# Optimization experiments

Measured on AMD Instinct MI355X. Metric: run time of the kernel, lower is better.

Reference implementation:

```python
import jax, jax.numpy as jnp
import numpy as np

B, D_IN, D_OUT = 16384, 2048, 2048
BN_EPS = 1e-5


def setup_inputs() -> dict:
    key = jax.random.key(0)
    ks = jax.random.split(key, 6)
    return {
        "x": jax.random.normal(ks[0], (B, D_IN), dtype=jnp.float32),
        "base_weight": jax.random.normal(ks[1], (D_OUT, D_IN), dtype=jnp.float32) * 0.1,
        "bias": jnp.zeros((D_OUT,), dtype=jnp.float32),
        "center": jax.random.normal(ks[2], (D_IN,), dtype=jnp.float32),
        "sharpness": jnp.ones((D_IN,), dtype=jnp.float32),
        "gamma": jnp.ones((D_OUT,), dtype=jnp.float32),
        "beta": jnp.zeros((D_OUT,), dtype=jnp.float32),
        "top_k": 256,
    }


def reference(x, base_weight, bias, center, sharpness, gamma, beta, top_k):
    # fuzzy membership: sigmoid(sharpness * (x - center))  -> [B, D_in]
    mu = jax.nn.sigmoid(sharpness * (x - center))
    b, d = mu.shape

    # OWA weighted membership: keep top_k memberships, scaled by
    # normalized linspace(1.0, 0.1, top_k) weights; zeros elsewhere.
    order = jnp.argsort(-mu, axis=1)                       # descending sort indices
    sorted_vals = jnp.take_along_axis(mu, order, axis=1)
    w = jnp.linspace(1.0, 0.1, top_k, dtype=mu.dtype)
    w = w / w.sum()
    owa = jnp.zeros_like(mu).at[
        jnp.arange(b)[:, None], order[:, :top_k]
    ].set(w[None, :] * sorted_vals[:, :top_k])

    # per-sample scaled matmul: bmm(W * mu_exp, x) == (owa * x) @ W^T
    out = (owa * x) @ base_weight.T + bias                 # [B, D_out]
    out = jax.nn.relu(out)

    # BatchNorm1d in training mode: batch mean, biased variance
    mean = out.mean(axis=0)
    var = out.var(axis=0)
    y = (out - mean) * jax.lax.rsqrt(var + BN_EPS) * gamma + beta
    return (y, mu)
```

## Files before the change

### kernel.cpp

```cpp
#include <hip/hip_runtime.h>
#include <stdint.h>

#define NB 16384
#define DI 2048
#define DO 2048
#define KTOP 256
#define LIST_CAP 384
#define MT (NB / 256)

typedef __attribute__((ext_vector_type(4))) float f32x4;
typedef __attribute__((ext_vector_type(8))) short s16x8;
typedef __attribute__((ext_vector_type(8))) unsigned short u16x8;

#define OWA_C0 7.10227273e-3f
#define OWA_C1 2.50668449e-5f

__device__ __forceinline__ ushort f2bf(float f) {
  uint32_t u = __float_as_uint(f);
  uint32_t r = (u + 0x7FFFu + ((u >> 16) & 1u)) >> 16;
  return (ushort)r;
}

__device__ __forceinline__ float bf2f(ushort b) {
  return __uint_as_float(((uint32_t)b) << 16);
}

__device__ __forceinline__ void gld_lds16(const void* g, void* l) {
  __builtin_amdgcn_global_load_lds((__attribute__((address_space(1))) void*)g,
                                   (__attribute__((address_space(3))) void*)l,
                                   16, 0, 0);
}

__global__ __launch_bounds__(256) void k_cvt(const float* __restrict__ W,
                                             ushort* __restrict__ Wb) {
  size_t i = ((size_t)blockIdx.x * 256 + threadIdx.x) * 8;
  float4 a = *(const float4*)(W + i);
  float4 b = *(const float4*)(W + i + 4);
  u16x8 o;
  o[0] = f2bf(a.x); o[1] = f2bf(a.y); o[2] = f2bf(a.z); o[3] = f2bf(a.w);
  o[4] = f2bf(b.x); o[5] = f2bf(b.y); o[6] = f2bf(b.z); o[7] = f2bf(b.w);
  *(u16x8*)(Wb + i) = o;
}

__global__ __launch_bounds__(256) void k_topk(
    const float* __restrict__ x, const float* __restrict__ center,
    const float* __restrict__ sharp, float* __restrict__ mu_out,
    ushort* __restrict__ A) {
  __shared__ __align__(16) float w_lds[DI];
  __shared__ uint32_t histR[8 * 256];
  __shared__ uint64_t list[LIST_CAP];
  __shared__ uint32_t babove[256];
  __shared__ uint32_t bcnt[256];
  __shared__ uint32_t pzero[256];
  __shared__ uint32_t scal[8];

  const int t = threadIdx.x;
  const int lane = t & 63;
  const int wv = t >> 6;
  const int row = blockIdx.x;
  const int base = t * 8;

  const float* xr = x + (size_t)row * DI + base;
  float4 xa = *(const float4*)(xr);
  float4 xb = *(const float4*)(xr + 4);
  float4 ca = *(const float4*)(center + base);
  float4 cb = *(const float4*)(center + base + 4);
  float4 sa = *(const float4*)(sharp + base);
  float4 sb = *(const float4*)(sharp + base + 4);

  float xv[8] = {xa.x, xa.y, xa.z, xa.w, xb.x, xb.y, xb.z, xb.w};
  float cv[8] = {ca.x, ca.y, ca.z, ca.w, cb.x, cb.y, cb.z, cb.w};
  float sv[8] = {sa.x, sa.y, sa.z, sa.w, sb.x, sb.y, sb.z, sb.w};
  float muv[8];
  uint32_t bits[8];
#pragma unroll
  for (int e = 0; e < 8; ++e) {
    float s = sv[e] * (xv[e] - cv[e]);
    float m = 1.0f / (1.0f + __expf(-s));
    muv[e] = m;
    bits[e] = __float_as_uint(m);
  }
  if (mu_out) {
    float4 m0; m0.x = muv[0]; m0.y = muv[1]; m0.z = muv[2]; m0.w = muv[3];
    float4 m1; m1.x = muv[4]; m1.y = muv[5]; m1.z = muv[6]; m1.w = muv[7];
    *(float4*)(mu_out + (size_t)row * DI + base) = m0;
    *(float4*)(mu_out + (size_t)row * DI + base + 4) = m1;
  }
  float4 z4; z4.x = z4.y = z4.z = z4.w = 0.f;
  *(float4*)(w_lds + base) = z4;
  *(float4*)(w_lds + base + 4) = z4;
  if (t == 0) scal[3] = 0;
#pragma unroll
  for (int i = 0; i < 8; ++i) histR[t + 256 * i] = 0;
  pzero[t] = 0;

  const uint32_t rep = (uint32_t)(t & 7) * 256u;

  uint32_t nhi = 0;
#pragma unroll
  for (int e = 0; e < 8; ++e) nhi += (bits[e] >> 24) == 0x3Fu;
#pragma unroll
  for (int off = 1; off < 64; off <<= 1) nhi += __shfl_xor(nhi, off);
  if (lane == 0) scal[4 + wv] = nhi;
  __syncthreads();
  const uint32_t c_hi = scal[4] + scal[5] + scal[6] + scal[7];

  uint32_t pfx = 0x3F000000u, krem = KTOP;
  if (c_hi < KTOP) {
#pragma unroll
    for (int e = 0; e < 8; ++e) atomicAdd(&histR[rep + (bits[e] >> 24)], 1u);
    __syncthreads();
    if (wv == 0) {
      uint32_t c0 = 0, c1 = 0, c2 = 0, c3 = 0;
#pragma unroll
      for (int r = 0; r < 8; ++r) {
        const uint32_t* h = &histR[r * 256 + lane * 4];
        c0 += h[0]; c1 += h[1]; c2 += h[2]; c3 += h[3];
      }
      uint32_t s3 = c3, s2 = c2 + s3, s1 = c1 + s2, s0 = c0 + s1;
      uint32_t Tl = s0, suf = s0;
#pragma unroll
      for (int off = 1; off < 64; off <<= 1) {
        uint32_t v = __shfl_down(suf, off);
        if (lane + off < 64) suf += v;
      }
      uint32_t above = suf - Tl;
      uint32_t SS[4] = {s0 + above, s1 + above, s2 + above, s3 + above};
      uint32_t cc[4] = {c0, c1, c2, c3};
#pragma unroll
      for (int j = 0; j < 4; ++j) {
        if (SS[j] >= KTOP && (SS[j] - cc[j]) < KTOP) {
          scal[0] = (uint32_t)(lane * 4 + j);
          scal[1] = SS[j] - cc[j];
        }
      }
    }
    __syncthreads();
    pfx = scal[0] << 24;
    krem = KTOP - scal[1];
#pragma unroll
    for (int i = 0; i < 8; ++i) histR[t + 256 * i] = 0;
    __syncthreads();
  }
  const uint32_t pfxbyte = pfx >> 24;
  const uint32_t nsuper = KTOP - krem;

#pragma unroll
  for (int e = 0; e < 8; ++e) {
    if ((bits[e] >> 24) == pfxbyte)
      atomicAdd(&histR[rep + ((bits[e] >> 16) & 255u)], 1u);
  }
  __syncthreads();
  if (wv == 0) {
    uint32_t c0 = 0, c1 = 0, c2 = 0, c3 = 0;
#pragma unroll
    for (int r = 0; r < 8; ++r) {
      const uint32_t* h = &histR[r * 256 + lane * 4];
      c0 += h[0]; c1 += h[1]; c2 += h[2]; c3 += h[3];
    }
    uint32_t s3 = c3, s2 = c2 + s3, s1 = c1 + s2, s0 = c0 + s1;
    uint32_t Tl = s0, suf = s0;
#pragma unroll
    for (int off = 1; off < 64; off <<= 1) {
      uint32_t v = __shfl_down(suf, off);
      if (lane + off < 64) suf += v;
    }
    uint32_t above = suf - Tl;
    uint32_t SS[4] = {s0 + above, s1 + above, s2 + above, s3 + above};
    uint32_t cc[4] = {c0, c1, c2, c3};
    uint4 ba, bc;
    ba.x = SS[0] - cc[0]; ba.y = SS[1] - cc[1];
    ba.z = SS[2] - cc[2]; ba.w = SS[3] - cc[3];
    bc.x = cc[0]; bc.y = cc[1]; bc.z = cc[2]; bc.w = cc[3];
    *(uint4*)&babove[lane * 4] = ba;
    *(uint4*)&bcnt[lane * 4] = bc;
#pragma unroll
    for (int j = 0; j < 4; ++j) {
      if (SS[j] >= krem && (SS[j] - cc[j]) < krem) {
        scal[0] = (uint32_t)(lane * 4 + j);
      }
    }
  }
  __syncthreads();
  const uint32_t tb = pfx | (scal[0] << 16);

  int lo8[8], hi8[8];
#pragma unroll
  for (int e = 0; e < 8; ++e) {
    lo8[e] = 0; hi8[e] = 0;
    if (bits[e] >= tb) {
      uint64_t key = ((uint64_t)bits[e] << 32) |
                     (uint64_t)(uint32_t)(DI - 1 - (base + e));
      uint32_t lo, hi, slot;
      if ((bits[e] >> 24) == pfxbyte) {
        uint32_t d = (bits[e] >> 16) & 255u;
        uint32_t idx = atomicAdd(&pzero[d], 1u);
        lo = nsuper + babove[d];
        hi = lo + bcnt[d];
        slot = lo + idx;
      } else {
        uint32_t idx = atomicAdd(&scal[3], 1u);
        lo = 0; hi = nsuper; slot = idx;
      }
      if (slot < LIST_CAP) list[slot] = key;
      lo8[e] = (int)lo;
      hi8[e] = (int)(hi > LIST_CAP ? LIST_CAP : hi);
    }
  }
  __syncthreads();

#pragma unroll
  for (int e = 0; e < 8; ++e) {
    if (bits[e] >= tb) {
      uint64_t key = ((uint64_t)bits[e] << 32) |
                     (uint64_t)(uint32_t)(DI - 1 - (base + e));
      int r = lo8[e];
      for (int j = lo8[e]; j < hi8[e]; ++j) r += (int)(list[j] > key);
      if (r < KTOP) w_lds[base + e] = OWA_C0 - OWA_C1 * (float)r;
    }
  }
  __syncthreads();

  u16x8 ov;
#pragma unroll
  for (int e = 0; e < 8; ++e) ov[e] = f2bf(w_lds[base + e] * muv[e] * xv[e]);
  *(u16x8*)(A + (size_t)row * DI + base) = ov;
}

#define HALFS 8192

#define MFMA(a, b, c) __builtin_amdgcn_mfma_f32_16x16x32_bf16(a, b, c, 0, 0, 0)

#define STAGE_A(U, h)                                                       \
  do {                                                                      \
    ushort* sl = lA + (((((U) & 1) << 1) + (h)) * HALFS);                   \
    gld_lds16(pA0 + (size_t)((h) * 128) * DI + (size_t)(U) * 64, sl + d0);  \
    gld_lds16(pA0 + (size_t)((h) * 128 + 64) * DI + (size_t)(U) * 64,       \
              sl + d1);                                                     \
  } while (0)

#define STAGE_B(U, h)                                                       \
  do {                                                                      \
    ushort* sl = lB + (((((U) & 1) << 1) + (h)) * HALFS);                   \
    gld_lds16(pB0 + (size_t)((h) * 128) * DI + (size_t)(U) * 64, sl + d0);  \
    gld_lds16(pB0 + (size_t)((h) * 128 + 64) * DI + (size_t)(U) * 64,       \
              sl + d1);                                                     \
  } while (0)

#define RD_A(BUF, slotp, rowb)                                              \
  do {                                                                      \
    const ushort* rp_ = (slotp) + ((rowb) + fr) * 64;                       \
    BUF[0] = *(const s16x8*)(rp_ + c0);                                     \
    BUF[1] = *(const s16x8*)(rp_ + c1);                                     \
    BUF[2] = *(const s16x8*)(rp_ + 16 * 64 + c0);                           \
    BUF[3] = *(const s16x8*)(rp_ + 16 * 64 + c1);                           \
  } while (0)

#define RD_B(slotp)                                                         \
  do {                                                                      \
    _Pragma("unroll") for (int ni = 0; ni < 4; ++ni) {                      \
      breg[ni][0] = *(const s16x8*)((slotp) + ni * 1024 + boff + c0);       \
      breg[ni][1] = *(const s16x8*)((slotp) + ni * 1024 + boff + c1);       \
    }                                                                       \
  } while (0)

#define MFMA_PHASE(q, BUF)                                                  \
  do {                                                                      \
    __builtin_amdgcn_s_setprio(1);                                          \
    _Pragma("unroll") for (int ni = 0; ni < 4; ++ni) {                      \
      acc[2 * (q)][ni] = MFMA(BUF[0], breg[ni][0], acc[2 * (q)][ni]);       \
      acc[2 * (q)][ni] = MFMA(BUF[1], breg[ni][1], acc[2 * (q)][ni]);       \
      acc[2 * (q) + 1][ni] = MFMA(BUF[2], breg[ni][0], acc[2 * (q) + 1][ni]); \
      acc[2 * (q) + 1][ni] = MFMA(BUF[3], breg[ni][1], acc[2 * (q) + 1][ni]); \
    }                                                                       \
    __builtin_amdgcn_s_setprio(0);                                          \
  } while (0)

#define PHASE(q, RD_STMT, STAGE_STMT, BUF, POST_STMT, TAIL_STMT, LG)        \
  do {                                                                      \
    RD_STMT;                                                                \
    STAGE_STMT;                                                             \
    asm volatile("s_waitcnt lgkmcnt(" LG ")" ::: "memory");                 \
    __builtin_amdgcn_sched_barrier(0);                                      \
    MFMA_PHASE(q, BUF);                                                     \
    POST_STMT;                                                              \
    TAIL_STMT;                                                              \
    __builtin_amdgcn_s_barrier();                                           \
  } while (0)

template <int OB16>
__global__ __launch_bounds__(512, 2) void k_gemm(
    const ushort* __restrict__ A, const ushort* __restrict__ Wb,
    const float* __restrict__ bias, float* __restrict__ outp,
    ushort* __restrict__ outb,
    float* __restrict__ psum, float* __restrict__ psumsq) {
  __shared__ __align__(16) ushort lA[4 * HALFS];
  __shared__ __align__(16) ushort lB[4 * HALFS];

  const int t = threadIdx.x;
  const int lane = t & 63;
  const int wv = t >> 6;
  const int wm = wv >> 2;
  const int wn = wv & 3;
  const int wm32 = wm * 32;
  const int fr = lane & 15;
  const int kg = lane >> 4;
  const int s = fr & 7;

  int bid = blockIdx.x;
  int orig = (bid & 7) * 64 + (bid >> 3);
  const int nb = orig & 7;
  const int mb = orig >> 3;
  const int m0 = mb * 256;
  const int n0 = nb * 256;

  const int srow0 = t >> 3;
  const int scol = ((t & 7) ^ (srow0 & 7)) * 8;
  const ushort* pA0 = A + (size_t)(m0 + srow0) * DI + scol;
  const ushort* pB0 = Wb + (size_t)(n0 + srow0) * DI + scol;
  const int d0 = t * 8;
  const int d1 = (512 + t) * 8;

  f32x4 acc[8][4];
#pragma unroll
  for (int i = 0; i < 8; ++i)
#pragma unroll
    for (int j = 0; j < 4; ++j) acc[i][j] = (f32x4){0.f, 0.f, 0.f, 0.f};

  const int c0 = (kg ^ s) * 8;
  const int c1 = ((4 + kg) ^ s) * 8;
  const int boff = ((wn & 1) * 64 + fr) * 64;

  s16x8 breg[4][2];
  s16x8 bufA_[4], bufB_[4];

  STAGE_B(0, 0); STAGE_B(0, 1);
  STAGE_A(0, 0); STAGE_A(0, 1);
  STAGE_B(1, 0); STAGE_B(1, 1);
  asm volatile("s_waitcnt vmcnt(6)" ::: "memory");
  __builtin_amdgcn_s_barrier();
  RD_B(lB + (wn >> 1) * HALFS);
  RD_A(bufA_, lA, wm32);

#pragma unroll 1
  for (int T = 0; T < 31; ++T) {
    const ushort* lAcur = lA + ((T & 1) << 1) * HALFS;
    const ushort* lAnxt = lA + (((T + 1) & 1) << 1) * HALFS;
    const ushort* sBnxt = lB + ((((T + 1) & 1) << 1) + (wn >> 1)) * HALFS;

    PHASE(0, RD_A(bufB_, lAcur, 64 + wm32), STAGE_A(T + 1, 0), bufA_, ,
          asm volatile("s_waitcnt vmcnt(6)" ::: "memory"), "4");
    PHASE(1, RD_A(bufA_, lAcur + HALFS, wm32), STAGE_A(T + 1, 1), bufB_, , ,
          "4");
    PHASE(2, RD_A(bufB_, lAcur + HALFS, 64 + wm32),
          if (T < 30) STAGE_B(T + 2, 0), bufA_, ,
          if (T < 30) { asm volatile("s_waitcnt vmcnt(4)" ::: "memory"); }
          else { asm volatile("s_waitcnt vmcnt(2)" ::: "memory"); }, "4");
    PHASE(3, RD_A(bufA_, lAnxt, wm32), if (T < 30) STAGE_B(T + 2, 1), bufB_,
          RD_B(sBnxt), , "4");
  }
  {
    const ushort* lAcur = lA + 2 * HALFS;
    PHASE(0, RD_A(bufB_, lAcur, 64 + wm32), , bufA_, ,
          asm volatile("s_waitcnt vmcnt(0)" ::: "memory"), "4");
    PHASE(1, RD_A(bufA_, lAcur + HALFS, wm32), , bufB_, , , "4");
    PHASE(2, RD_A(bufB_, lAcur + HALFS, 64 + wm32), , bufA_, , , "4");
    PHASE(3, , , bufB_, , , "0");
  }

  __syncthreads();
  float* colsum = (float*)lA;
  float* colsq = colsum + 256;
  if (t < 256) { colsum[t] = 0.f; colsq[t] = 0.f; }
  __syncthreads();
#pragma unroll
  for (int ni = 0; ni < 4; ++ni) {
    const int n = n0 + wn * 64 + ni * 16 + fr;
    const float bv = bias[n];
    float cs = 0.f, cq = 0.f;
#pragma unroll
    for (int mi = 0; mi < 8; ++mi) {
      const int rowb = m0 + 64 * (mi >> 1) + wm32 + 16 * (mi & 1) + kg * 4;
      f32x4 v = acc[mi][ni];
#pragma unroll
      for (int r = 0; r < 4; ++r) {
        float zz = fmaxf(v[r] + bv, 0.f);
        if (OB16) outb[(size_t)(rowb + r) * DO + n] = f2bf(zz);
        else      outp[(size_t)(rowb + r) * DO + n] = zz;
        cs += zz;
        cq += zz * zz;
      }
    }
    cs += __shfl_xor(cs, 16); cq += __shfl_xor(cq, 16);
    cs += __shfl_xor(cs, 32); cq += __shfl_xor(cq, 32);
    if (kg == 0) {
      atomicAdd(&colsum[wn * 64 + ni * 16 + fr], cs);
      atomicAdd(&colsq[wn * 64 + ni * 16 + fr], cq);
    }
  }
  __syncthreads();
  if (t < 256) {
    psum[(size_t)mb * DO + n0 + t] = colsum[t];
    psumsq[(size_t)mb * DO + n0 + t] = colsq[t];
  }
}

__global__ __launch_bounds__(256) void k_bnfin(
    const float* __restrict__ psum, const float* __restrict__ psumsq,
    const float* __restrict__ gamma, const float* __restrict__ beta,
    float* __restrict__ scaleA, float* __restrict__ shiftA) {
  int n = blockIdx.x * 256 + threadIdx.x;
  float s = 0.f, q = 0.f;
  for (int r = 0; r < MT; ++r) {
    s += psum[(size_t)r * DO + n];
    q += psumsq[(size_t)r * DO + n];
  }
  float mean = s * (1.0f / (float)NB);
  float var = q * (1.0f / (float)NB) - mean * mean;
  var = fmaxf(var, 0.f);
  float rstd = rsqrtf(var + 1e-5f);
  float sc = gamma[n] * rstd;
  scaleA[n] = sc;
  shiftA[n] = beta[n] - mean * sc;
}

__global__ __launch_bounds__(256) void k_bnapply(float* __restrict__ outp,
                                                 const float* __restrict__ scaleA,
                                                 const float* __restrict__ shiftA) {
  size_t i = ((size_t)blockIdx.x * 256 + threadIdx.x) * 4;
  int n = (int)(i & (DO - 1));
  float4 v = *(float4*)(outp + i);
  float4 sc = *(const float4*)(scaleA + n);
  float4 sh = *(const float4*)(shiftA + n);
  v.x = v.x * sc.x + sh.x;
  v.y = v.y * sc.y + sh.y;
  v.z = v.z * sc.z + sh.z;
  v.w = v.w * sc.w + sh.w;
  *(float4*)(outp + i) = v;
}

__global__ __launch_bounds__(256) void k_bnapply_b16(
    const ushort* __restrict__ outb, float* __restrict__ y,
    const float* __restrict__ scaleA, const float* __restrict__ shiftA) {
  size_t i = ((size_t)blockIdx.x * 256 + threadIdx.x) * 8;
  int n = (int)(i & (DO - 1));
  u16x8 v = *(const u16x8*)(outb + i);
  float4 s0 = *(const float4*)(scaleA + n);
  float4 s1 = *(const float4*)(scaleA + n + 4);
  float4 h0 = *(const float4*)(shiftA + n);
  float4 h1 = *(const float4*)(shiftA + n + 4);
  float4 y0, y1;
  y0.x = bf2f(v[0]) * s0.x + h0.x;
  y0.y = bf2f(v[1]) * s0.y + h0.y;
  y0.z = bf2f(v[2]) * s0.z + h0.z;
  y0.w = bf2f(v[3]) * s0.w + h0.w;
  y1.x = bf2f(v[4]) * s1.x + h1.x;
  y1.y = bf2f(v[5]) * s1.y + h1.y;
  y1.z = bf2f(v[6]) * s1.z + h1.z;
  y1.w = bf2f(v[7]) * s1.w + h1.w;
  *(float4*)(y + i) = y0;
  *(float4*)(y + i + 4) = y1;
}

__global__ __launch_bounds__(256) void k_mu(const float* __restrict__ x,
                                            const float* __restrict__ center,
                                            const float* __restrict__ sharp,
                                            float* __restrict__ mu_out) {
  const int t = threadIdx.x;
  const int row = blockIdx.x;
  const int base = t * 8;
  const float* xr = x + (size_t)row * DI + base;
  float4 xa = *(const float4*)(xr);
  float4 xb = *(const float4*)(xr + 4);
  float4 ca = *(const float4*)(center + base);
  float4 cb = *(const float4*)(center + base + 4);
  float4 sa = *(const float4*)(sharp + base);
  float4 sb = *(const float4*)(sharp + base + 4);
  float xv[8] = {xa.x, xa.y, xa.z, xa.w, xb.x, xb.y, xb.z, xb.w};
  float cv[8] = {ca.x, ca.y, ca.z, ca.w, cb.x, cb.y, cb.z, cb.w};
  float sv[8] = {sa.x, sa.y, sa.z, sa.w, sb.x, sb.y, sb.z, sb.w};
  float mu[8];
#pragma unroll
  for (int e = 0; e < 8; ++e) {
    float s = sv[e] * (xv[e] - cv[e]);
    mu[e] = 1.0f / (1.0f + __expf(-s));
  }
  float4 m0; m0.x = mu[0]; m0.y = mu[1]; m0.z = mu[2]; m0.w = mu[3];
  float4 m1; m1.x = mu[4]; m1.y = mu[5]; m1.z = mu[6]; m1.w = mu[7];
  *(float4*)(mu_out + (size_t)row * DI + base) = m0;
  *(float4*)(mu_out + (size_t)row * DI + base + 4) = m1;
}

extern "C" void kernel_launch(void* const* d_in, const int* in_sizes, int n_in,
                              void* d_out, int out_size, void* d_ws, size_t ws_size,
                              hipStream_t stream) {
  (void)in_sizes; (void)n_in; (void)out_size;
  const float* x = (const float*)d_in[0];
  const float* W = (const float*)d_in[1];
  const float* bias = (const float*)d_in[2];
  const float* center = (const float*)d_in[3];
  const float* sharp = (const float*)d_in[4];
  const float* gamma = (const float*)d_in[5];
  const float* beta = (const float*)d_in[6];

  float* outY = (float*)d_out;
  float* outMu = outY + (size_t)NB * DO;

  const size_t A_BYTES = (size_t)NB * DI * 2;
  const size_t WB_BYTES = (size_t)DO * DI * 2;
  const size_t PS_BYTES = (size_t)MT * DO * 4;
  const size_t SC_BYTES = (size_t)DO * 4;
  const size_t OB_BYTES = (size_t)NB * DO * 2;
  const size_t NEED_BIG = A_BYTES + WB_BYTES + 2 * PS_BYTES + 2 * SC_BYTES;

  char* p = (char*)d_ws;
  bool bigws = (ws_size >= NEED_BIG);
  bool ob16 = (ws_size >= NEED_BIG + OB_BYTES);
  ushort* A;
  if (bigws) { A = (ushort*)p; p += A_BYTES; }
  else       { A = (ushort*)outMu; }
  ushort* Wb = (ushort*)p; p += WB_BYTES;
  float* psum = (float*)p; p += PS_BYTES;
  float* psumsq = (float*)p; p += PS_BYTES;
  float* scaleA = (float*)p; p += SC_BYTES;
  float* shiftA = (float*)p; p += SC_BYTES;
  ushort* outB = (ushort*)p;

  k_cvt<<<dim3((DO * DI) / (256 * 8)), dim3(256), 0, stream>>>(W, Wb);
  k_topk<<<dim3(NB), dim3(256), 0, stream>>>(x, center, sharp,
                                             bigws ? outMu : (float*)nullptr, A);
  if (ob16) {
    k_gemm<1><<<dim3((NB / 256) * (DO / 256)), dim3(512), 0, stream>>>(
        A, Wb, bias, outY, outB, psum, psumsq);
  } else {
    k_gemm<0><<<dim3((NB / 256) * (DO / 256)), dim3(512), 0, stream>>>(
        A, Wb, bias, outY, (ushort*)outY , psum, psumsq);
  }
  k_bnfin<<<dim3(DO / 256), dim3(256), 0, stream>>>(psum, psumsq, gamma, beta,
                                                    scaleA, shiftA);
  if (ob16) {
    k_bnapply_b16<<<dim3((size_t)NB * DO / 8 / 256), dim3(256), 0, stream>>>(
        outB, outY, scaleA, shiftA);
  } else {
    k_bnapply<<<dim3((size_t)NB * DO / 4 / 256), dim3(256), 0, stream>>>(
        outY, scaleA, shiftA);
  }
  if (!bigws) k_mu<<<dim3(NB), dim3(256), 0, stream>>>(x, center, sharp, outMu);
}
```

Measured before the change: 305.8 us.

## Split GEMM tile across 16 waves with 1024-thread blocks

Doubles the GEMM workgroup from 512 to 1024 threads, so each wave computes a 16-row by 64-column slice with half the accumulators and A fragments. Each thread now issues one global-to-LDS load per stage instead of two, and the wait counts are adjusted to match. Column statistics now go into per-wave-row slots in LDS and are summed at the end instead of using LDS atomics. Each phase gains an extra barrier and a full lgkmcnt(0) wait before its MFMAs, which drops the previous A-fragment double-buffering. Occupancy falls to one block per CU, so there is less latency hiding and more synchronisation.

```diff
diff --git a/kernel.cpp b/kernel.cpp
--- a/kernel.cpp
+++ b/kernel.cpp
@@ -235,25 +235,19 @@
   do {                                                                      \
     ushort* sl = lA + (((((U) & 1) << 1) + (h)) * HALFS);                   \
     gld_lds16(pA0 + (size_t)((h) * 128) * DI + (size_t)(U) * 64, sl + d0);  \
-    gld_lds16(pA0 + (size_t)((h) * 128 + 64) * DI + (size_t)(U) * 64,       \
-              sl + d1);                                                     \
   } while (0)
 
 #define STAGE_B(U, h)                                                       \
   do {                                                                      \
     ushort* sl = lB + (((((U) & 1) << 1) + (h)) * HALFS);                   \
     gld_lds16(pB0 + (size_t)((h) * 128) * DI + (size_t)(U) * 64, sl + d0);  \
-    gld_lds16(pB0 + (size_t)((h) * 128 + 64) * DI + (size_t)(U) * 64,       \
-              sl + d1);                                                     \
   } while (0)
 
-#define RD_A(BUF, slotp, rowb)                                              \
+#define RD_A(slotp, rowb)                                                   \
   do {                                                                      \
     const ushort* rp_ = (slotp) + ((rowb) + fr) * 64;                       \
-    BUF[0] = *(const s16x8*)(rp_ + c0);                                     \
-    BUF[1] = *(const s16x8*)(rp_ + c1);                                     \
-    BUF[2] = *(const s16x8*)(rp_ + 16 * 64 + c0);                           \
-    BUF[3] = *(const s16x8*)(rp_ + 16 * 64 + c1);                           \
+    abuf[0] = *(const s16x8*)(rp_ + c0);                                    \
+    abuf[1] = *(const s16x8*)(rp_ + c1);                                    \
   } while (0)
 
 #define RD_B(slotp)                                                         \
@@ -264,32 +258,31 @@
     }                                                                       \
   } while (0)
 
-#define MFMA_PHASE(q, BUF)                                                  \
+#define MFMA_PHASE(q)                                                       \
   do {                                                                      \
     __builtin_amdgcn_s_setprio(1);                                          \
     _Pragma("unroll") for (int ni = 0; ni < 4; ++ni) {                      \
-      acc[2 * (q)][ni] = MFMA(BUF[0], breg[ni][0], acc[2 * (q)][ni]);       \
-      acc[2 * (q)][ni] = MFMA(BUF[1], breg[ni][1], acc[2 * (q)][ni]);       \
-      acc[2 * (q) + 1][ni] = MFMA(BUF[2], breg[ni][0], acc[2 * (q) + 1][ni]); \
-      acc[2 * (q) + 1][ni] = MFMA(BUF[3], breg[ni][1], acc[2 * (q) + 1][ni]); \
+      acc[q][ni] = MFMA(abuf[0], breg[ni][0], acc[q][ni]);                  \
+      acc[q][ni] = MFMA(abuf[1], breg[ni][1], acc[q][ni]);                  \
     }                                                                       \
     __builtin_amdgcn_s_setprio(0);                                          \
   } while (0)
 
-#define PHASE(q, RD_STMT, STAGE_STMT, BUF, POST_STMT, TAIL_STMT, LG)        \
+#define PHASE(q, RD_STMT, STAGE_STMT, POST_STMT, TAIL_STMT)                 \
   do {                                                                      \
     RD_STMT;                                                                \
     STAGE_STMT;                                                             \
-    asm volatile("s_waitcnt lgkmcnt(" LG ")" ::: "memory");                 \
+    __builtin_amdgcn_s_barrier();                                           \
+    asm volatile("s_waitcnt lgkmcnt(0)" ::: "memory");                      \
     __builtin_amdgcn_sched_barrier(0);                                      \
-    MFMA_PHASE(q, BUF);                                                     \
+    MFMA_PHASE(q);                                                          \
     POST_STMT;                                                              \
     TAIL_STMT;                                                              \
     __builtin_amdgcn_s_barrier();                                           \
   } while (0)
 
 template <int OB16>
-__global__ __launch_bounds__(512, 2) void k_gemm(
+__global__ __launch_bounds__(1024) void k_gemm(
     const ushort* __restrict__ A, const ushort* __restrict__ Wb,
     const float* __restrict__ bias, float* __restrict__ outp,
     ushort* __restrict__ outb,
@@ -302,7 +295,7 @@
   const int wv = t >> 6;
   const int wm = wv >> 2;
   const int wn = wv & 3;
-  const int wm32 = wm * 32;
+  const int wm16 = wm * 16;
   const int fr = lane & 15;
   const int kg = lane >> 4;
   const int s = fr & 7;
@@ -319,11 +312,10 @@
   const ushort* pA0 = A + (size_t)(m0 + srow0) * DI + scol;
   const ushort* pB0 = Wb + (size_t)(n0 + srow0) * DI + scol;
   const int d0 = t * 8;
-  const int d1 = (512 + t) * 8;
-
-  f32x4 acc[8][4];
-#pragma unroll
-  for (int i = 0; i < 8; ++i)
+
+  f32x4 acc[4][4];
+#pragma unroll
+  for (int i = 0; i < 4; ++i)
 #pragma unroll
     for (int j = 0; j < 4; ++j) acc[i][j] = (f32x4){0.f, 0.f, 0.f, 0.f};
 
@@ -332,46 +324,43 @@
   const int boff = ((wn & 1) * 64 + fr) * 64;
 
   s16x8 breg[4][2];
-  s16x8 bufA_[4], bufB_[4];
+  s16x8 abuf[2];
 
   STAGE_B(0, 0); STAGE_B(0, 1);
   STAGE_A(0, 0); STAGE_A(0, 1);
   STAGE_B(1, 0); STAGE_B(1, 1);
-  asm volatile("s_waitcnt vmcnt(6)" ::: "memory");
+  asm volatile("s_waitcnt vmcnt(3)" ::: "memory");
   __builtin_amdgcn_s_barrier();
   RD_B(lB + (wn >> 1) * HALFS);
-  RD_A(bufA_, lA, wm32);
 
 #pragma unroll 1
   for (int T = 0; T < 31; ++T) {
     const ushort* lAcur = lA + ((T & 1) << 1) * HALFS;
-    const ushort* lAnxt = lA + (((T + 1) & 1) << 1) * HALFS;
     const ushort* sBnxt = lB + ((((T + 1) & 1) << 1) + (wn >> 1)) * HALFS;
 
-    PHASE(0, RD_A(bufB_, lAcur, 64 + wm32), STAGE_A(T + 1, 0), bufA_, ,
-          asm volatile("s_waitcnt vmcnt(6)" ::: "memory"), "4");
-    PHASE(1, RD_A(bufA_, lAcur + HALFS, wm32), STAGE_A(T + 1, 1), bufB_, , ,
-          "4");
-    PHASE(2, RD_A(bufB_, lAcur + HALFS, 64 + wm32),
-          if (T < 30) STAGE_B(T + 2, 0), bufA_, ,
-          if (T < 30) { asm volatile("s_waitcnt vmcnt(4)" ::: "memory"); }
-          else { asm volatile("s_waitcnt vmcnt(2)" ::: "memory"); }, "4");
-    PHASE(3, RD_A(bufA_, lAnxt, wm32), if (T < 30) STAGE_B(T + 2, 1), bufB_,
-          RD_B(sBnxt), , "4");
+    PHASE(0, RD_A(lAcur, wm16), STAGE_A(T + 1, 0), ,
+          asm volatile("s_waitcnt vmcnt(3)" ::: "memory"));
+    PHASE(1, RD_A(lAcur, 64 + wm16), STAGE_A(T + 1, 1), , );
+    PHASE(2, RD_A(lAcur + HALFS, wm16), if (T < 30) STAGE_B(T + 2, 0), ,
+          if (T < 30) { asm volatile("s_waitcnt vmcnt(2)" ::: "memory"); }
+          else { asm volatile("s_waitcnt vmcnt(1)" ::: "memory"); });
+    PHASE(3, RD_A(lAcur + HALFS, 64 + wm16), if (T < 30) STAGE_B(T + 2, 1),
+          RD_B(sBnxt), );
   }
   {
     const ushort* lAcur = lA + 2 * HALFS;
-    PHASE(0, RD_A(bufB_, lAcur, 64 + wm32), , bufA_, ,
-          asm volatile("s_waitcnt vmcnt(0)" ::: "memory"), "4");
-    PHASE(1, RD_A(bufA_, lAcur + HALFS, wm32), , bufB_, , , "4");
-    PHASE(2, RD_A(bufB_, lAcur + HALFS, 64 + wm32), , bufA_, , , "4");
-    PHASE(3, , , bufB_, , , "0");
-  }
-
-  __syncthreads();
-  float* colsum = (float*)lA;
-  float* colsq = colsum + 256;
-  if (t < 256) { colsum[t] = 0.f; colsq[t] = 0.f; }
+    PHASE(0, RD_A(lAcur, wm16), , ,
+          asm volatile("s_waitcnt vmcnt(0)" ::: "memory"));
+    PHASE(1, RD_A(lAcur, 64 + wm16), , , );
+    PHASE(2, RD_A(lAcur + HALFS, wm16), , , );
+    PHASE(3, RD_A(lAcur + HALFS, 64 + wm16), , , );
+  }
+
+  __syncthreads();
+  float* csum = (float*)lA;
+  float* csq = csum + 1024;
+  csum[t & 1023] = 0.f;
+  csq[t & 1023] = 0.f;
   __syncthreads();
 #pragma unroll
   for (int ni = 0; ni < 4; ++ni) {
@@ -379,8 +368,8 @@
     const float bv = bias[n];
     float cs = 0.f, cq = 0.f;
 #pragma unroll
-    for (int mi = 0; mi < 8; ++mi) {
-      const int rowb = m0 + 64 * (mi >> 1) + wm32 + 16 * (mi & 1) + kg * 4;
+    for (int mi = 0; mi < 4; ++mi) {
+      const int rowb = m0 + 64 * mi + wm16 + kg * 4;
       f32x4 v = acc[mi][ni];
 #pragma unroll
       for (int r = 0; r < 4; ++r) {
@@ -394,14 +383,16 @@
     cs += __shfl_xor(cs, 16); cq += __shfl_xor(cq, 16);
     cs += __shfl_xor(cs, 32); cq += __shfl_xor(cq, 32);
     if (kg == 0) {
-      atomicAdd(&colsum[wn * 64 + ni * 16 + fr], cs);
-      atomicAdd(&colsq[wn * 64 + ni * 16 + fr], cq);
+      csum[wm * 256 + wn * 64 + ni * 16 + fr] = cs;
+      csq[wm * 256 + wn * 64 + ni * 16 + fr] = cq;
     }
   }
   __syncthreads();
   if (t < 256) {
-    psum[(size_t)mb * DO + n0 + t] = colsum[t];
-    psumsq[(size_t)mb * DO + n0 + t] = colsq[t];
+    float s4 = csum[t] + csum[256 + t] + csum[512 + t] + csum[768 + t];
+    float q4 = csq[t] + csq[256 + t] + csq[512 + t] + csq[768 + t];
+    psum[(size_t)mb * DO + n0 + t] = s4;
+    psumsq[(size_t)mb * DO + n0 + t] = q4;
   }
 }
 
@@ -530,10 +521,10 @@
   k_topk<<<dim3(NB), dim3(256), 0, stream>>>(x, center, sharp,
                                              bigws ? outMu : (float*)nullptr, A);
   if (ob16) {
-    k_gemm<1><<<dim3((NB / 256) * (DO / 256)), dim3(512), 0, stream>>>(
+    k_gemm<1><<<dim3((NB / 256) * (DO / 256)), dim3(1024), 0, stream>>>(
         A, Wb, bias, outY, outB, psum, psumsq);
   } else {
-    k_gemm<0><<<dim3((NB / 256) * (DO / 256)), dim3(512), 0, stream>>>(
+    k_gemm<0><<<dim3((NB / 256) * (DO / 256)), dim3(1024), 0, stream>>>(
         A, Wb, bias, outY, (ushort*)outY , psum, psumsq);
   }
   k_bnfin<<<dim3(DO / 256), dim3(256), 0, stream>>>(psum, psumsq, gamma, beta,
```

After: 325.9 us. +6.6%, slower.
